# Kernel tuning notes

Measured on AMD Instinct MI355X. Metric: run time of the kernel, lower is better.

## Reference

```python
import jax, jax.numpy as jnp
import numpy as np

N, D_IN, HID, OUT, E = 131072, 256, 1024, 1, 100


def setup_inputs() -> dict:
    key = jax.random.key(0)
    k = jax.random.split(key, 7)
    return {
        "x": jax.random.normal(k[0], (N, D_IN), dtype=jnp.float32),
        "W1": jax.random.normal(k[1], (HID, D_IN), dtype=jnp.float32) * 0.05,
        "b1": jax.random.normal(k[2], (HID,), dtype=jnp.float32) * 0.05,
        "We": jax.random.normal(k[3], (E, OUT, HID), dtype=jnp.float32) * 0.05,
        "be": jax.random.normal(k[4], (E, OUT), dtype=jnp.float32) * 0.05,
        "num": jax.random.randint(k[5], (N,), 0, E, dtype=jnp.int64),
        "c": jax.random.randint(k[6], (E,), 0, E, dtype=jnp.int64),
    }


def reference(x, W1, b1, We, be, num, c):
    # feature: Linear + ReLU  -> [N, HID]
    h = jax.nn.relu(x @ W1.T + b1)
    # per-sample expert index: c[num[i]]
    e = c[num]                                  # [N]
    Wg = We[e]                                  # [N, OUT, HID] gathered expert weights
    bg = be[e]                                  # [N, OUT]
    y = jnp.einsum('noh,nh->no', Wg, h) + bg    # per-sample expert linear
    return jax.nn.sigmoid(y)
```

## Files before the change

kernel.cpp:

```cpp
#include <hip/hip_runtime.h>
#include <stdint.h>

#define N_SAMP 131072
#define DIN    256
#define HIDN   1024
#define BROWS  128
#define NCHUNK 16

typedef __attribute__((ext_vector_type(8))) short short8;
typedef __attribute__((ext_vector_type(4))) float f32x4;

__device__ __forceinline__ unsigned short f2bf(float f) {
  unsigned u = __float_as_uint(f);
  u += 0x7fffu + ((u >> 16) & 1u);
  return (unsigned short)(u >> 16);
}

__device__ __forceinline__ short8 pack8(float4 a, float4 b) {
  short8 r;
  r[0] = (short)f2bf(a.x); r[1] = (short)f2bf(a.y);
  r[2] = (short)f2bf(a.z); r[3] = (short)f2bf(a.w);
  r[4] = (short)f2bf(b.x); r[5] = (short)f2bf(b.y);
  r[6] = (short)f2bf(b.z); r[7] = (short)f2bf(b.w);
  return r;
}

__global__ __launch_bounds__(256) void w1_to_bf16(const float* __restrict__ W1,
                                                  unsigned short* __restrict__ o) {
  int i = blockIdx.x * 256 + threadIdx.x;
  float4 f = ((const float4*)W1)[i];
  ushort4 v;
  v.x = f2bf(f.x); v.y = f2bf(f.y); v.z = f2bf(f.z); v.w = f2bf(f.w);
  ((ushort4*)o)[i] = v;
}

template <bool WBF>
__global__ __launch_bounds__(256, 2) void fused_kernel(
    const float* __restrict__ x,
    const float* __restrict__ W1f,
    const unsigned short* __restrict__ W1b,
    const float* __restrict__ b1,
    const float* __restrict__ We,
    const float* __restrict__ be,
    const int* __restrict__ num,
    const int* __restrict__ c,
    float* __restrict__ out)
{
  __shared__ unsigned short Wt[2][64 * DIN];
  __shared__ int e_sh[BROWS];

  const int tid  = threadIdx.x;
  const int lane = tid & 63;
  const int w    = tid >> 6;
  const int n    = lane & 15;
  const int quad = lane >> 4;
  const int R0   = blockIdx.x * BROWS;

  if (tid < BROWS) e_sh[tid] = c[num[R0 + tid]];

  short8 afr[2][8];
  {
    const float* xr0 = x + (size_t)(R0 + w * 32 + n) * DIN + quad * 8;
#pragma unroll
    for (int t = 0; t < 2; ++t) {
      const float* xr = xr0 + (size_t)t * 16 * DIN;
#pragma unroll
      for (int s = 0; s < 8; ++s) {
        float4 f0 = *(const float4*)(xr + s * 32);
        float4 f1 = *(const float4*)(xr + s * 32 + 4);
        afr[t][s] = pack8(f0, f1);
      }
    }
  }

  const int h2 = lane >> 5;
  const int p  = lane & 31;

  if (WBF) {
#pragma unroll
    for (int j = 0; j < 8; ++j) {
      int inst = w * 8 + j;
      int r = inst * 2 + h2;
      int kg = p ^ ((r & 7) << 2);
      const unsigned short* g = W1b + (r << 8) + (kg << 3);
      __builtin_amdgcn_global_load_lds(
          (const __attribute__((address_space(1))) unsigned int*)g,
          (__attribute__((address_space(3))) unsigned int*)(&Wt[0][0] + inst * 512),
          16, 0, 0);
    }
  } else {
#pragma unroll
    for (int j = 0; j < 8; ++j) {
      int id = tid + j * 256;
      int r = id >> 5, pp = id & 31;
      int kg = pp ^ ((r & 7) << 2);
      const float* gs = W1f + (r << 8) + (kg << 3);
      float4 f0 = *(const float4*)gs;
      float4 f1 = *(const float4*)(gs + 4);
      *(short8*)&Wt[0][r * DIN + pp * 8] = pack8(f0, f1);
    }
  }

  __syncthreads();

  int eoff[2][4];
#pragma unroll
  for (int t = 0; t < 2; ++t)
#pragma unroll
    for (int r = 0; r < 4; ++r)
      eoff[t][r] = e_sh[w * 32 + t * 16 + quad * 4 + r] * HIDN;

  float yacc[2][4] = {{0.f, 0.f, 0.f, 0.f}, {0.f, 0.f, 0.f, 0.f}};

  int buf = 0;
  for (int ch = 0; ch < NCHUNK; ++ch) {
    if (ch + 1 < NCHUNK) {
      if (WBF) {
        const unsigned short* Wg = W1b + (size_t)(ch + 1) * (64 * DIN);
        unsigned short* db = &Wt[buf ^ 1][0];
#pragma unroll
        for (int j = 0; j < 8; ++j) {
          int inst = w * 8 + j;
          int r = inst * 2 + h2;
          int kg = p ^ ((r & 7) << 2);
          const unsigned short* g = Wg + (r << 8) + (kg << 3);
          __builtin_amdgcn_global_load_lds(
              (const __attribute__((address_space(1))) unsigned int*)g,
              (__attribute__((address_space(3))) unsigned int*)(db + inst * 512),
              16, 0, 0);
        }
      } else {
        const float* Wg = W1f + (size_t)(ch + 1) * (64 * DIN);
#pragma unroll
        for (int j = 0; j < 8; ++j) {
          int id = tid + j * 256;
          int r = id >> 5, pp = id & 31;
          int kg = pp ^ ((r & 7) << 2);
          const float* gs = Wg + (r << 8) + (kg << 3);
          float4 f0 = *(const float4*)gs;
          float4 f1 = *(const float4*)(gs + 4);
          *(short8*)&Wt[buf ^ 1][r * DIN + pp * 8] = pack8(f0, f1);
        }
      }
    }

    const unsigned short* WtB = &Wt[buf][0];
    f32x4 acc[2][4];
#pragma unroll
    for (int t = 0; t < 2; ++t)
#pragma unroll
      for (int nt = 0; nt < 4; ++nt)
        acc[t][nt] = (f32x4){0.f, 0.f, 0.f, 0.f};

#pragma unroll
    for (int s = 0; s < 8; ++s) {
      const int F = (s * 4 + quad) ^ ((n & 7) << 2);
      short8 bfr[4];
#pragma unroll
      for (int nt = 0; nt < 4; ++nt)
        bfr[nt] = *(const short8*)&WtB[(nt * 16 + n) * DIN + F * 8];
#pragma unroll
      for (int t = 0; t < 2; ++t)
#pragma unroll
        for (int nt = 0; nt < 4; ++nt)
          acc[t][nt] = __builtin_amdgcn_mfma_f32_16x16x32_bf16(
              afr[t][s], bfr[nt], acc[t][nt], 0, 0, 0);
    }

#pragma unroll
    for (int nt = 0; nt < 4; ++nt) {
      int col = ch * 64 + nt * 16 + n;
      float bv = b1[col];
      const float* Wec = We + col;
#pragma unroll
      for (int t = 0; t < 2; ++t)
#pragma unroll
        for (int r = 0; r < 4; ++r) {
          float h = acc[t][nt][r] + bv;
          h = fmaxf(h, 0.f);
          yacc[t][r] = fmaf(h, Wec[eoff[t][r]], yacc[t][r]);
        }
    }

    __syncthreads();
    buf ^= 1;
  }

#pragma unroll
  for (int t = 0; t < 2; ++t)
#pragma unroll
    for (int r = 0; r < 4; ++r) {
      float v = yacc[t][r];
      v += __shfl_xor(v, 1);
      v += __shfl_xor(v, 2);
      v += __shfl_xor(v, 4);
      v += __shfl_xor(v, 8);
      yacc[t][r] = v;
    }

  if (n == 0) {
#pragma unroll
    for (int t = 0; t < 2; ++t)
#pragma unroll
      for (int r = 0; r < 4; ++r) {
        int row = R0 + w * 32 + t * 16 + quad * 4 + r;
        float yy = yacc[t][r] + be[eoff[t][r] >> 10];
        out[row] = 1.f / (1.f + __expf(-yy));
      }
  }
}

extern "C" void kernel_launch(void* const* d_in, const int* in_sizes, int n_in,
                              void* d_out, int out_size, void* d_ws, size_t ws_size,
                              hipStream_t stream) {
  const float* x   = (const float*)d_in[0];
  const float* W1  = (const float*)d_in[1];
  const float* b1  = (const float*)d_in[2];
  const float* We  = (const float*)d_in[3];
  const float* be  = (const float*)d_in[4];
  const int*   num = (const int*)d_in[5];
  const int*   c   = (const int*)d_in[6];
  float* out = (float*)d_out;

  const size_t w1bf_bytes = (size_t)HIDN * DIN * sizeof(unsigned short);
  const bool usebf = ws_size >= w1bf_bytes;
  unsigned short* w1bf = (unsigned short*)d_ws;

  if (usebf) {
    w1_to_bf16<<<dim3((HIDN * DIN / 4) / 256), dim3(256), 0, stream>>>(W1, w1bf);
    fused_kernel<true><<<dim3(N_SAMP / BROWS), dim3(256), 0, stream>>>(
        x, W1, w1bf, b1, We, be, num, c, out);
  } else {
    fused_kernel<false><<<dim3(N_SAMP / BROWS), dim3(256), 0, stream>>>(
        x, W1, w1bf, b1, We, be, num, c, out);
  }
}
```

Baseline: 261.0 us.

## Double rows per block to halve W1 reloads, split N-tiles into halves

Each block now processes 256 rows instead of 128, with every wave holding four 16-row A tiles instead of two. The per-chunk MFMA loop is split into two halves of two N-tiles each, which keeps the accumulator count the same while the A fragments double. This halves the number of blocks and the total W1 streaming through LDS, so each loaded B fragment is reused across more rows. The costs are more register pressure from the larger afr, eoff and yacc arrays, and fewer blocks (512) to fill the GPU.

```diff
diff --git a/kernel.cpp b/kernel.cpp
--- a/kernel.cpp
+++ b/kernel.cpp
@@ -4,7 +4,8 @@
 #define N_SAMP 131072
 #define DIN    256
 #define HIDN   1024
-#define BROWS  128
+#define BROWS  256
+#define NTHREADS 256
 #define NCHUNK 16
 
 typedef __attribute__((ext_vector_type(8))) short short8;
@@ -35,7 +36,7 @@
 }
 
 template <bool WBF>
-__global__ __launch_bounds__(256, 2) void fused_kernel(
+__global__ __launch_bounds__(NTHREADS, 2) void fused_kernel(
     const float* __restrict__ x,
     const float* __restrict__ W1f,
     const unsigned short* __restrict__ W1b,
@@ -58,11 +59,11 @@
 
   if (tid < BROWS) e_sh[tid] = c[num[R0 + tid]];
 
-  short8 afr[2][8];
+  short8 afr[4][8];
   {
-    const float* xr0 = x + (size_t)(R0 + w * 32 + n) * DIN + quad * 8;
-#pragma unroll
-    for (int t = 0; t < 2; ++t) {
+    const float* xr0 = x + (size_t)(R0 + w * 64 + n) * DIN + quad * 8;
+#pragma unroll
+    for (int t = 0; t < 4; ++t) {
       const float* xr = xr0 + (size_t)t * 16 * DIN;
 #pragma unroll
       for (int s = 0; s < 8; ++s) {
@@ -91,7 +92,7 @@
   } else {
 #pragma unroll
     for (int j = 0; j < 8; ++j) {
-      int id = tid + j * 256;
+      int id = tid + j * NTHREADS;
       int r = id >> 5, pp = id & 31;
       int kg = pp ^ ((r & 7) << 2);
       const float* gs = W1f + (r << 8) + (kg << 3);
@@ -103,14 +104,18 @@
 
   __syncthreads();
 
-  int eoff[2][4];
-#pragma unroll
-  for (int t = 0; t < 2; ++t)
+  int eoff[4][4];
+#pragma unroll
+  for (int t = 0; t < 4; ++t)
 #pragma unroll
     for (int r = 0; r < 4; ++r)
-      eoff[t][r] = e_sh[w * 32 + t * 16 + quad * 4 + r] * HIDN;
-
-  float yacc[2][4] = {{0.f, 0.f, 0.f, 0.f}, {0.f, 0.f, 0.f, 0.f}};
+      eoff[t][r] = e_sh[w * 64 + t * 16 + quad * 4 + r] * HIDN;
+
+  float yacc[4][4];
+#pragma unroll
+  for (int t = 0; t < 4; ++t)
+#pragma unroll
+    for (int r = 0; r < 4; ++r) yacc[t][r] = 0.f;
 
   int buf = 0;
   for (int ch = 0; ch < NCHUNK; ++ch) {
@@ -133,7 +138,7 @@
         const float* Wg = W1f + (size_t)(ch + 1) * (64 * DIN);
 #pragma unroll
         for (int j = 0; j < 8; ++j) {
-          int id = tid + j * 256;
+          int id = tid + j * NTHREADS;
           int r = id >> 5, pp = id & 31;
           int kg = pp ^ ((r & 7) << 2);
           const float* gs = Wg + (r << 8) + (kg << 3);
@@ -145,41 +150,45 @@
     }
 
     const unsigned short* WtB = &Wt[buf][0];
-    f32x4 acc[2][4];
-#pragma unroll
-    for (int t = 0; t < 2; ++t)
-#pragma unroll
-      for (int nt = 0; nt < 4; ++nt)
-        acc[t][nt] = (f32x4){0.f, 0.f, 0.f, 0.f};
-
-#pragma unroll
-    for (int s = 0; s < 8; ++s) {
-      const int F = (s * 4 + quad) ^ ((n & 7) << 2);
-      short8 bfr[4];
-#pragma unroll
-      for (int nt = 0; nt < 4; ++nt)
-        bfr[nt] = *(const short8*)&WtB[(nt * 16 + n) * DIN + F * 8];
-#pragma unroll
-      for (int t = 0; t < 2; ++t)
-#pragma unroll
-        for (int nt = 0; nt < 4; ++nt)
-          acc[t][nt] = __builtin_amdgcn_mfma_f32_16x16x32_bf16(
-              afr[t][s], bfr[nt], acc[t][nt], 0, 0, 0);
-    }
-
-#pragma unroll
-    for (int nt = 0; nt < 4; ++nt) {
-      int col = ch * 64 + nt * 16 + n;
-      float bv = b1[col];
-      const float* Wec = We + col;
-#pragma unroll
-      for (int t = 0; t < 2; ++t)
-#pragma unroll
-        for (int r = 0; r < 4; ++r) {
-          float h = acc[t][nt][r] + bv;
-          h = fmaxf(h, 0.f);
-          yacc[t][r] = fmaf(h, Wec[eoff[t][r]], yacc[t][r]);
-        }
+
+#pragma unroll
+    for (int half = 0; half < 2; ++half) {
+      f32x4 acc[4][2];
+#pragma unroll
+      for (int t = 0; t < 4; ++t)
+#pragma unroll
+        for (int nn = 0; nn < 2; ++nn)
+          acc[t][nn] = (f32x4){0.f, 0.f, 0.f, 0.f};
+
+#pragma unroll
+      for (int s = 0; s < 8; ++s) {
+        const int F = (s * 4 + quad) ^ ((n & 7) << 2);
+        short8 bfr[2];
+#pragma unroll
+        for (int nn = 0; nn < 2; ++nn)
+          bfr[nn] = *(const short8*)&WtB[((half * 2 + nn) * 16 + n) * DIN + F * 8];
+#pragma unroll
+        for (int t = 0; t < 4; ++t)
+#pragma unroll
+          for (int nn = 0; nn < 2; ++nn)
+            acc[t][nn] = __builtin_amdgcn_mfma_f32_16x16x32_bf16(
+                afr[t][s], bfr[nn], acc[t][nn], 0, 0, 0);
+      }
+
+#pragma unroll
+      for (int nn = 0; nn < 2; ++nn) {
+        int col = ch * 64 + (half * 2 + nn) * 16 + n;
+        float bv = b1[col];
+        const float* Wec = We + col;
+#pragma unroll
+        for (int t = 0; t < 4; ++t)
+#pragma unroll
+          for (int r = 0; r < 4; ++r) {
+            float h = acc[t][nn][r] + bv;
+            h = fmaxf(h, 0.f);
+            yacc[t][r] = fmaf(h, Wec[eoff[t][r]], yacc[t][r]);
+          }
+      }
     }
 
     __syncthreads();
@@ -187,7 +196,7 @@
   }
 
 #pragma unroll
-  for (int t = 0; t < 2; ++t)
+  for (int t = 0; t < 4; ++t)
 #pragma unroll
     for (int r = 0; r < 4; ++r) {
       float v = yacc[t][r];
@@ -200,10 +209,10 @@
 
   if (n == 0) {
 #pragma unroll
-    for (int t = 0; t < 2; ++t)
+    for (int t = 0; t < 4; ++t)
 #pragma unroll
       for (int r = 0; r < 4; ++r) {
-        int row = R0 + w * 32 + t * 16 + quad * 4 + r;
+        int row = R0 + w * 64 + t * 16 + quad * 4 + r;
         float yy = yacc[t][r] + be[eoff[t][r] >> 10];
         out[row] = 1.f / (1.f + __expf(-yy));
       }
@@ -228,10 +237,10 @@
 
   if (usebf) {
     w1_to_bf16<<<dim3((HIDN * DIN / 4) / 256), dim3(256), 0, stream>>>(W1, w1bf);
-    fused_kernel<true><<<dim3(N_SAMP / BROWS), dim3(256), 0, stream>>>(
+    fused_kernel<true><<<dim3(N_SAMP / BROWS), dim3(NTHREADS), 0, stream>>>(
         x, W1, w1bf, b1, We, be, num, c, out);
   } else {
-    fused_kernel<false><<<dim3(N_SAMP / BROWS), dim3(256), 0, stream>>>(
+    fused_kernel<false><<<dim3(N_SAMP / BROWS), dim3(NTHREADS), 0, stream>>>(
         x, W1, w1bf, b1, We, be, num, c, out);
   }
 }
```

New measurement: 456.4 us. 74.8% more time.
